# Kernel optimization log

Hardware: AMD Instinct MI355X
Metric: run time of the kernel (lower is better)

The kernel has to match this reference:

```python
import jax, jax.numpy as jnp
import numpy as np

DIM = 384
KEY_DIM = 32
NUM_HEADS = 8
ATTN_RATIO = 4
RESOLUTION = 48
N_TOKENS = RESOLUTION * RESOLUTION  # 2304
D_V = ATTN_RATIO * KEY_DIM          # 128
NH_KD = NUM_HEADS * KEY_DIM         # 256
DH = NUM_HEADS * D_V                # 1024
SCALE = KEY_DIM ** (-0.5)


def _make_bias_idxs(res):
    # offset (|dy|,|dx|) -> unique id via dy*res+dx (bijection onto 0..res^2-1)
    coords = np.stack(np.meshgrid(np.arange(res), np.arange(res), indexing='ij'), -1).reshape(-1, 2)
    off = np.abs(coords[:, None, :] - coords[None, :, :])  # (N,N,2)
    return (off[..., 0] * res + off[..., 1]).astype(np.int32)  # (N,N)


def setup_inputs() -> dict:
    key = jax.random.key(0)
    ks = jax.random.split(key, 12)
    f32 = jnp.float32
    x = jax.random.normal(ks[0], (N_TOKENS, DIM, 1, 1), dtype=f32)
    # 1x1 convs == linear layers: weight (out, in), bias (out,)
    q_w = jax.random.normal(ks[1], (NH_KD, DIM), dtype=f32) * 0.05
    q_b = jax.random.normal(ks[2], (NH_KD,), dtype=f32) * 0.02
    k_w = jax.random.normal(ks[3], (NH_KD, DIM), dtype=f32) * 0.05
    k_b = jax.random.normal(ks[4], (NH_KD,), dtype=f32) * 0.02
    v_w = jax.random.normal(ks[5], (DH, DIM), dtype=f32) * 0.05
    v_b = jax.random.normal(ks[6], (DH,), dtype=f32) * 0.02
    proj_w = jax.random.normal(ks[7], (DIM, DH), dtype=f32) * 0.05
    proj_b = jax.random.normal(ks[8], (DIM,), dtype=f32) * 0.02
    attention_biases = jax.random.normal(ks[9], (NUM_HEADS, 1, RESOLUTION * RESOLUTION), dtype=f32) * 0.02
    bias_idxs = jnp.asarray(_make_bias_idxs(RESOLUTION))  # (N,N) int32
    return {
        'x': x, 'q_w': q_w, 'q_b': q_b, 'k_w': k_w, 'k_b': k_b,
        'v_w': v_w, 'v_b': v_b, 'proj_w': proj_w, 'proj_b': proj_b,
        'attention_biases': attention_biases, 'bias_idxs': bias_idxs,
    }


def reference(x, q_w, q_b, k_w, k_b, v_w, v_b, proj_w, proj_b, attention_biases, bias_idxs):
    N = x.shape[0]
    xf = x.reshape(N, DIM)  # H=W=1 so 1x1 conv is a matmul
    q = (xf @ q_w.T + q_b).reshape(N, NUM_HEADS, KEY_DIM).transpose(1, 0, 2)  # (H,N,kd)
    k = (xf @ k_w.T + k_b).reshape(N, NUM_HEADS, KEY_DIM).transpose(1, 0, 2)  # (H,N,kd)
    v = (xf @ v_w.T + v_b).reshape(N, NUM_HEADS, D_V).transpose(1, 0, 2)      # (H,N,dv)
    bias = attention_biases[:, 0, :][:, bias_idxs]  # gather -> (H,N,N)
    attn = jnp.einsum('hnd,hmd->hnm', q, k) * SCALE + bias
    attn = jax.nn.softmax(attn, axis=-1)
    out = jnp.einsum('hnm,hmd->hnd', attn, v)       # (H,N,dv)
    out = out.transpose(1, 0, 2).reshape(N, DH)
    y = out @ proj_w.T + proj_b
    return y.reshape(N, DIM, 1, 1)
```

## Files before the change

kernel.cpp:

```cpp
#include <hip/hip_runtime.h>

typedef unsigned short u16;
typedef unsigned int u32;
typedef short bf16x8 __attribute__((ext_vector_type(8)));
typedef float f32x4 __attribute__((ext_vector_type(4)));

#define SCALE 0.17677669529663687f

static __device__ __forceinline__ float bf2f(u16 h) {
    u32 u = ((u32)h) << 16;
    float f;
    __builtin_memcpy(&f, &u, 4);
    return f;
}
static __device__ __forceinline__ u16 f2bf(float f) {
    u32 u;
    __builtin_memcpy(&u, &f, 4);
    u += 0x7fffu + ((u >> 16) & 1u);
    return (u16)(u >> 16);
}
static __device__ __forceinline__ float IN1(const void* p, int idx, int md) {
    return md ? ((const float*)p)[idx] : bf2f(((const u16*)p)[idx]);
}

__global__ void detect_kernel(const unsigned int* __restrict__ x, int* __restrict__ mode)
{
    int lane = threadIdx.x;
    int cnt = 0;
    for (int i = lane; i < 4096; i += 64) {
        unsigned int e = (x[i] >> 7) & 0xFFu;
        cnt += (e >= 100u && e <= 140u) ? 1 : 0;
    }
    for (int off = 32; off; off >>= 1) cnt += __shfl_down(cnt, off);
    if (lane == 0) *mode = (cnt < 2048) ? 1 : 0;
}

struct ConvArgs {
    const void* src[9];
    int ofs[10];
};
__global__ __launch_bounds__(256) void convert_all(
    ConvArgs a, u16* __restrict__ dst, const int* __restrict__ mode, int total)
{
    const int md = *mode;
    int base = (blockIdx.x * 256 + threadIdx.x) * 8;
    for (int e = 0; e < 8; e++) {
        int i = base + e;
        if (i >= total) return;
        int t = 0;
        for (int j = 1; j < 9; j++) t += (i >= a.ofs[j]) ? 1 : 0;
        int idx = i - a.ofs[t];
        dst[i] = md ? f2bf(((const float*)a.src[t])[idx])
                    : ((const u16*)a.src[t])[idx];
    }
}

__global__ __launch_bounds__(256) void qkv_kernel(
    const u16* __restrict__ x,
    const u16* __restrict__ qw, const u16* __restrict__ qb,
    const u16* __restrict__ kw, const u16* __restrict__ kb,
    const u16* __restrict__ vw, const u16* __restrict__ vb,
    u16* __restrict__ qo, u16* __restrict__ kT, u16* __restrict__ vTt)
{
    __shared__ __align__(16) short As[64 * 72];
    __shared__ __align__(16) short Bs[128 * 72];
    __shared__ __align__(16) short outS[128 * 72];
    const int tid  = threadIdx.x;
    const int lane = tid & 63;
    const int w    = tid >> 6;
    const int l15  = lane & 15, quad = lane >> 4;
    const int mT = blockIdx.y, nT = blockIdx.x;

    const u16* wp; const u16* bp; int r0, which;
    if (nT < 2)      { wp = qw; bp = qb; r0 = nT * 128;       which = 0; }
    else if (nT < 4) { wp = kw; bp = kb; r0 = (nT - 2) * 128; which = 1; }
    else             { wp = vw; bp = vb; r0 = (nT - 4) * 128; which = 2; }

    const int wm = (w >> 1) * 32, wn = (w & 1) * 64;
    const f32x4 vz = {0.f, 0.f, 0.f, 0.f};
    f32x4 acc[2][4];
    for (int mi = 0; mi < 2; mi++)
        for (int ni = 0; ni < 4; ni++) acc[mi][ni] = vz;

    const int arow = tid >> 2, aseg = tid & 3;
    const int brow = tid >> 1, bseg = tid & 1;

    for (int kk = 0; kk < 384; kk += 64) {
        for (int c = 0; c < 2; c++)
            *(bf16x8*)&As[arow * 72 + aseg * 16 + c * 8] =
                *(const bf16x8*)&x[(mT * 64 + arow) * 384 + kk + aseg * 16 + c * 8];
        for (int c = 0; c < 4; c++)
            *(bf16x8*)&Bs[brow * 72 + bseg * 32 + c * 8] =
                *(const bf16x8*)&wp[(r0 + brow) * 384 + kk + bseg * 32 + c * 8];
        __syncthreads();
        for (int s = 0; s < 2; s++) {
            bf16x8 af[2], bfr[4];
            for (int mi = 0; mi < 2; mi++)
                af[mi] = *(const bf16x8*)&As[(wm + mi * 16 + l15) * 72 + s * 32 + quad * 8];
            for (int ni = 0; ni < 4; ni++)
                bfr[ni] = *(const bf16x8*)&Bs[(wn + ni * 16 + l15) * 72 + s * 32 + quad * 8];
            for (int mi = 0; mi < 2; mi++)
                for (int ni = 0; ni < 4; ni++)
                    acc[mi][ni] = __builtin_amdgcn_mfma_f32_16x16x32_bf16(
                        af[mi], bfr[ni], acc[mi][ni], 0, 0, 0);
        }
        __syncthreads();
    }

    for (int ni = 0; ni < 4; ni++) {
        int colL = wn + ni * 16 + l15;
        float bias = bf2f(bp[r0 + colL]);
        for (int mi = 0; mi < 2; mi++) {
            int tokb = wm + mi * 16 + quad * 4;
            for (int rr = 0; rr < 4; rr++) {
                u16 val = f2bf(acc[mi][ni][rr] + bias);
                if (which == 2) outS[colL * 72 + tokb + rr] = val;
                else            outS[(tokb + rr) * 136 + colL] = val;
            }
        }
    }
    __syncthreads();

    if (which == 0) {
        for (int i = 0; i < 4; i++) {
            int c = tid + i * 256;
            int tok = c >> 4, seg = c & 15;
            *(bf16x8*)&qo[(mT * 64 + tok) * 256 + r0 + seg * 8] =
                *(const bf16x8*)&outS[tok * 136 + seg * 8];
        }
    } else if (which == 1) {
        int h0 = r0 >> 5;
        for (int i = 0; i < 4; i++) {
            int c = tid + i * 256;
            int tile = c >> 6, ln = c & 63;
            int head_loc = tile >> 2, t16_loc = tile & 3;
            int q2 = ln >> 4, l2 = ln & 15;
            *(bf16x8*)&kT[(((h0 + head_loc) * 144 + mT * 4 + t16_loc) << 9) + ln * 8] =
                *(const bf16x8*)&outS[(t16_loc * 16 + l2) * 136 + head_loc * 32 + q2 * 8];
        }
    } else {
        int hv = r0 >> 7;
        for (int i = 0; i < 4; i++) {
            int c = tid + i * 256;
            int tile = c >> 6, ln = c & 63;
            int kt_loc = tile >> 3, vb2 = tile & 7;
            int q2 = ln >> 4, l2 = ln & 15;
            *(bf16x8*)&vTt[(((hv * 72 + mT * 2 + kt_loc) * 8 + vb2) << 9) + ln * 8] =
                *(const bf16x8*)&outS[(vb2 * 16 + l2) * 72 + kt_loc * 32 + q2 * 8];
        }
    }
}

__global__ __launch_bounds__(256) void attn_v6(
    const u16* __restrict__ qbuf, const u16* __restrict__ kT,
    const u16* __restrict__ vTt,  const void* __restrict__ ab,
    u16* __restrict__ obuf, const int* __restrict__ mode)
{
    __shared__ __align__(16) float abl[2304];
    __shared__ __align__(16) u16   Pl[4][2][640];
    __shared__ __align__(16) float osh[2048];
    __shared__ __align__(16) float lsh[16];

    const int tid  = threadIdx.x;
    const int lane = tid & 63;
    const int w    = tid >> 6;
    const int l15  = lane & 15, quad = lane >> 4;
    const int head = blockIdx.y;
    const int q0   = blockIdx.x * 16;
    const int md   = *mode;

    for (int i = tid; i < 2304; i += 256) abl[i] = IN1(ab, head * 2304 + i, md);
    for (int i = tid; i < 2048; i += 256) osh[i] = 0.f;
    if (tid < 16) lsh[tid] = 0.f;
    __syncthreads();

    bf16x8 qfrag = *(const bf16x8*)&qbuf[(q0 + l15) * 256 + head * 32 + quad * 8];

    int qr[4], qc[4];
    for (int r = 0; r < 4; r++) {
        int qrow = q0 + quad * 4 + r;
        qr[r] = qrow / 48; qc[r] = qrow % 48;
    }

    const f32x4 vz = {0.f, 0.f, 0.f, 0.f};
    f32x4 o[8];
    for (int vb = 0; vb < 8; vb++) o[vb] = vz;
    float ls[4] = {0.f, 0.f, 0.f, 0.f};

    const int kstart = w * 576;
    const u16* kTb = kT  + head * 73728;
    const u16* vTb = vTt + head * 294912;
    const int t16 = kstart >> 4;
    const int vt0 = kstart >> 5;

    auto score_step = [&](int tt, bf16x8 a0, bf16x8 a1) {
        int kb = kstart + tt * 32;
        f32x4 s0 = __builtin_amdgcn_mfma_f32_16x16x32_bf16(qfrag, a0, vz, 0, 0, 0);
        f32x4 s1 = __builtin_amdgcn_mfma_f32_16x16x32_bf16(qfrag, a1, vz, 0, 0, 0);
        int k0 = kb + l15, k1 = k0 + 16;
        int kr0 = k0 / 48, kc0 = k0 % 48;
        int kr1 = k1 / 48, kc1 = k1 % 48;
        u16* P = &Pl[w][tt & 1][0];
        for (int r = 0; r < 4; r++) {
            float a0f = s0[r] * SCALE + abl[abs(qr[r] - kr0) * 48 + abs(qc[r] - kc0)];
            a0f = fminf(fmaxf(a0f, -60.f), 60.f);
            float p0 = __expf(a0f);
            ls[r] += p0;
            P[(quad * 4 + r) * 40 + l15] = f2bf(p0);
            float a1f = s1[r] * SCALE + abl[abs(qr[r] - kr1) * 48 + abs(qc[r] - kc1)];
            a1f = fminf(fmaxf(a1f, -60.f), 60.f);
            float p1 = __expf(a1f);
            ls[r] += p1;
            P[(quad * 4 + r) * 40 + 16 + l15] = f2bf(p1);
        }
    };

    {
        bf16x8 c0 = *(const bf16x8*)&kTb[((t16 + 0) * 64 + lane) * 8];
        bf16x8 c1 = *(const bf16x8*)&kTb[((t16 + 1) * 64 + lane) * 8];
        score_step(0, c0, c1);
    }
    bf16x8 kA0 = *(const bf16x8*)&kTb[((t16 + 2) * 64 + lane) * 8];
    bf16x8 kA1 = *(const bf16x8*)&kTb[((t16 + 3) * 64 + lane) * 8];

    for (int t = 0; t < 18; t++) {
        bf16x8 pf = *(const bf16x8*)&Pl[w][t & 1][l15 * 40 + quad * 8];

        bf16x8 vf[8];
        for (int vb = 0; vb < 8; vb++)
            vf[vb] = *(const bf16x8*)&vTb[(((vt0 + t) * 8 + vb) * 64 + lane) * 8];

        if (t < 17) {
            int nt = (t + 2 <= 17) ? (t + 2) : 17;
            bf16x8 kB0 = *(const bf16x8*)&kTb[((t16 + nt * 2) * 64 + lane) * 8];
            bf16x8 kB1 = *(const bf16x8*)&kTb[((t16 + nt * 2 + 1) * 64 + lane) * 8];
            score_step(t + 1, kA0, kA1);
            kA0 = kB0; kA1 = kB1;
        }

        for (int vb = 0; vb < 8; vb++)
            o[vb] = __builtin_amdgcn_mfma_f32_16x16x32_bf16(pf, vf[vb], o[vb], 0, 0, 0);
    }

    for (int r = 0; r < 4; r++)
        for (int off = 1; off < 16; off <<= 1)
            ls[r] += __shfl_xor(ls[r], off);

    for (int ph = 0; ph < 4; ph++) {
        if (w == ph) {
            for (int vb = 0; vb < 8; vb++)
                for (int r = 0; r < 4; r++)
                    osh[(quad * 4 + r) * 128 + vb * 16 + l15] += o[vb][r];
            if (l15 == 0)
                for (int r = 0; r < 4; r++) lsh[quad * 4 + r] += ls[r];
        }
        __syncthreads();
    }

    for (int i = tid; i < 2048; i += 256) {
        int row = i >> 7, dv = i & 127;
        obuf[(q0 + row) * 1024 + head * 128 + dv] = f2bf(osh[i] / lsh[row]);
    }
}

__global__ __launch_bounds__(256) void proj_kernel(
    const u16* __restrict__ ob, const u16* __restrict__ pw,
    const u16* __restrict__ pb, void* __restrict__ y, const int* __restrict__ mode)
{
    __shared__ __align__(16) short As[64 * 136];
    __shared__ __align__(16) short Bs[64 * 136];
    const int tid  = threadIdx.x;
    const int lane = tid & 63;
    const int w    = tid >> 6;
    const int l15  = lane & 15, quad = lane >> 4;
    const int mT = blockIdx.y, nT = blockIdx.x;
    const int wm = (w >> 1) * 32, wn = (w & 1) * 32;
    const int md = *mode;

    const f32x4 vz = {0.f, 0.f, 0.f, 0.f};
    f32x4 acc[2][2];
    for (int mi = 0; mi < 2; mi++)
        for (int ni = 0; ni < 2; ni++) acc[mi][ni] = vz;

    const int row = tid >> 2, seg = tid & 3;
    for (int kk = 0; kk < 1024; kk += 128) {
        for (int c = 0; c < 4; c++) {
            *(bf16x8*)&As[row * 136 + seg * 32 + c * 8] =
                *(const bf16x8*)&ob[(mT * 64 + row) * 1024 + kk + seg * 32 + c * 8];
            *(bf16x8*)&Bs[row * 136 + seg * 32 + c * 8] =
                *(const bf16x8*)&pw[(nT * 64 + row) * 1024 + kk + seg * 32 + c * 8];
        }
        __syncthreads();
        for (int s = 0; s < 4; s++) {
            bf16x8 af[2], bfr[2];
            for (int mi = 0; mi < 2; mi++)
                af[mi] = *(const bf16x8*)&As[(wm + mi * 16 + l15) * 136 + s * 32 + quad * 8];
            for (int ni = 0; ni < 2; ni++)
                bfr[ni] = *(const bf16x8*)&Bs[(wn + ni * 16 + l15) * 136 + s * 32 + quad * 8];
            for (int mi = 0; mi < 2; mi++)
                for (int ni = 0; ni < 2; ni++)
                    acc[mi][ni] = __builtin_amdgcn_mfma_f32_16x16x32_bf16(
                        af[mi], bfr[ni], acc[mi][ni], 0, 0, 0);
        }
        __syncthreads();
    }

    for (int ni = 0; ni < 2; ni++) {
        int col = nT * 64 + wn + ni * 16 + l15;
        float bias = bf2f(pb[col]);
        for (int mi = 0; mi < 2; mi++) {
            int rowb = mT * 64 + wm + mi * 16 + quad * 4;
            for (int rr = 0; rr < 4; rr++) {
                float val = acc[mi][ni][rr] + bias;
                int idx = (rowb + rr) * 384 + col;
                if (md) ((float*)y)[idx] = val;
                else    ((u16*)y)[idx]   = f2bf(val);
            }
        }
    }
}

extern "C" void kernel_launch(void* const* d_in, const int* in_sizes, int n_in,
                              void* d_out, int out_size, void* d_ws, size_t ws_size,
                              hipStream_t stream)
{
    const void *x = 0, *qw = 0, *qb = 0, *kw = 0, *kb = 0;
    const void *vw = 0, *vb = 0, *pw = 0, *pb = 0, *ab = 0;
    void* scratch = 0;

    for (int i = 0; i < n_in; i++) {
        const void* p = d_in[i];
        switch (in_sizes[i]) {
            case 884736:  x  = p; break;
            case 98304:   if (!qw) qw = p; else kw = p; break;
            case 256:     if (!qb) qb = p; else kb = p; break;
            case 393216:  if (!vw) vw = p; else pw = p; break;
            case 1024:    vb = p; break;
            case 384:     pb = p; break;
            case 18432:   ab = p; break;
            case 5308416: scratch = (void*)p; break;
        }
    }
    if (!scratch) scratch = d_ws;

    u16* arena = (u16*)scratch;
    u16* cx  = arena;
    u16* cqw = arena + 884736;
    u16* cqb = arena + 983040;
    u16* ckw = arena + 983296;
    u16* ckb = arena + 1081600;
    u16* cvw = arena + 1081856;
    u16* cvb = arena + 1475072;
    u16* cpw = arena + 1476096;
    u16* cpb = arena + 1869312;
    u16* q_bf = arena + 1869696;
    u16* kT   = arena + 2459520;
    u16* vTt  = arena + 3049344;
    u16* ob   = arena + 7767936;
    int* mode = ((int*)scratch) + 5308400;

    detect_kernel<<<1, 64, 0, stream>>>((const unsigned int*)x, mode);

    ConvArgs ca;
    ca.src[0] = x;  ca.src[1] = qw; ca.src[2] = qb; ca.src[3] = kw; ca.src[4] = kb;
    ca.src[5] = vw; ca.src[6] = vb; ca.src[7] = pw; ca.src[8] = pb;
    ca.ofs[0] = 0;       ca.ofs[1] = 884736;  ca.ofs[2] = 983040;
    ca.ofs[3] = 983296;  ca.ofs[4] = 1081600; ca.ofs[5] = 1081856;
    ca.ofs[6] = 1475072; ca.ofs[7] = 1476096; ca.ofs[8] = 1869312;
    ca.ofs[9] = 1869696;
    convert_all<<<(1869696 / 8 + 255) / 256, 256, 0, stream>>>(ca, arena, mode, 1869696);

    qkv_kernel<<<dim3(12, 36), 256, 0, stream>>>(cx, cqw, cqb, ckw, ckb, cvw, cvb,
                                                 q_bf, kT, vTt);
    attn_v6<<<dim3(144, 8), 256, 0, stream>>>(q_bf, kT, vTt, ab, ob, mode);
    proj_kernel<<<dim3(6, 36), 256, 0, stream>>>(ob, cpw, cpb, d_out, mode);
}
```

Baseline: 171.4 us.

## Fold dtype detection into convert, double-buffer QKV GEMM, use exp2 softmax

Removes the separate detect kernel by having every convert block recompute the dtype check on the first 1024 words of x, with block 0 writing the mode flag for later kernels. Double-buffers the QKV GEMM's LDS tiles through register prefetch so global loads overlap the MFMAs, with one barrier per k-step instead of two. In attention, the bias table is stored as bf16 pre-scaled by log2e and the score exponent uses exp2 with a folded scale, dropping the clamp. This saves a launch and softmax ALU work, at the cost of extra LDS, slightly lower bias precision, and possible overflow without the clamp since no max is subtracted.

```diff
diff --git a/kernel.cpp b/kernel.cpp
--- a/kernel.cpp
+++ b/kernel.cpp
@@ -5,7 +5,14 @@
 typedef short bf16x8 __attribute__((ext_vector_type(8)));
 typedef float f32x4 __attribute__((ext_vector_type(4)));
 
-#define SCALE 0.17677669529663687f
+#define SCALE2 0.25505413f
+#define LOG2E  1.4426950408889634f
+
+#if __has_builtin(__builtin_amdgcn_exp2f)
+#define EXP2(x) __builtin_amdgcn_exp2f(x)
+#else
+#define EXP2(x) exp2f(x)
+#endif
 
 static __device__ __forceinline__ float bf2f(u16 h) {
     u32 u = ((u32)h) << 16;
@@ -23,26 +30,28 @@
     return md ? ((const float*)p)[idx] : bf2f(((const u16*)p)[idx]);
 }
 
-__global__ void detect_kernel(const unsigned int* __restrict__ x, int* __restrict__ mode)
-{
-    int lane = threadIdx.x;
-    int cnt = 0;
-    for (int i = lane; i < 4096; i += 64) {
-        unsigned int e = (x[i] >> 7) & 0xFFu;
-        cnt += (e >= 100u && e <= 140u) ? 1 : 0;
-    }
-    for (int off = 32; off; off >>= 1) cnt += __shfl_down(cnt, off);
-    if (lane == 0) *mode = (cnt < 2048) ? 1 : 0;
-}
-
 struct ConvArgs {
     const void* src[9];
     int ofs[10];
 };
 __global__ __launch_bounds__(256) void convert_all(
-    ConvArgs a, u16* __restrict__ dst, const int* __restrict__ mode, int total)
-{
-    const int md = *mode;
+    ConvArgs a, u16* __restrict__ dst, int* __restrict__ mode_out, int total)
+{
+    __shared__ int cnt_sh;
+    if (threadIdx.x == 0) cnt_sh = 0;
+    __syncthreads();
+    const u32* xw = (const u32*)a.src[0];
+    int c = 0;
+    for (int i = threadIdx.x; i < 1024; i += 256) {
+        u32 e = (xw[i] >> 7) & 0xFFu;
+        c += (e >= 100u && e <= 140u) ? 1 : 0;
+    }
+    for (int off = 32; off; off >>= 1) c += __shfl_down(c, off);
+    if ((threadIdx.x & 63) == 0) atomicAdd(&cnt_sh, c);
+    __syncthreads();
+    const int md = (cnt_sh < 512) ? 1 : 0;
+    if (blockIdx.x == 0 && threadIdx.x == 0) *mode_out = md;
+
     int base = (blockIdx.x * 256 + threadIdx.x) * 8;
     for (int e = 0; e < 8; e++) {
         int i = base + e;
@@ -62,8 +71,8 @@
     const u16* __restrict__ vw, const u16* __restrict__ vb,
     u16* __restrict__ qo, u16* __restrict__ kT, u16* __restrict__ vTt)
 {
-    __shared__ __align__(16) short As[64 * 72];
-    __shared__ __align__(16) short Bs[128 * 72];
+    __shared__ __align__(16) short As[2][64 * 72];
+    __shared__ __align__(16) short Bs[2][128 * 72];
     __shared__ __align__(16) short outS[128 * 72];
     const int tid  = threadIdx.x;
     const int lane = tid & 63;
@@ -85,27 +94,44 @@
     const int arow = tid >> 2, aseg = tid & 3;
     const int brow = tid >> 1, bseg = tid & 1;
 
-    for (int kk = 0; kk < 384; kk += 64) {
+    bf16x8 ra[2], rb[4];
+    auto load_tile = [&](int kk) {
         for (int c = 0; c < 2; c++)
-            *(bf16x8*)&As[arow * 72 + aseg * 16 + c * 8] =
-                *(const bf16x8*)&x[(mT * 64 + arow) * 384 + kk + aseg * 16 + c * 8];
+            ra[c] = *(const bf16x8*)&x[(mT * 64 + arow) * 384 + kk + aseg * 16 + c * 8];
         for (int c = 0; c < 4; c++)
-            *(bf16x8*)&Bs[brow * 72 + bseg * 32 + c * 8] =
-                *(const bf16x8*)&wp[(r0 + brow) * 384 + kk + bseg * 32 + c * 8];
-        __syncthreads();
+            rb[c] = *(const bf16x8*)&wp[(r0 + brow) * 384 + kk + bseg * 32 + c * 8];
+    };
+    auto store_tile = [&](int b) {
+        for (int c = 0; c < 2; c++)
+            *(bf16x8*)&As[b][arow * 72 + aseg * 16 + c * 8] = ra[c];
+        for (int c = 0; c < 4; c++)
+            *(bf16x8*)&Bs[b][brow * 72 + bseg * 32 + c * 8] = rb[c];
+    };
+
+    load_tile(0);
+    store_tile(0);
+    __syncthreads();
+
+    for (int t = 0; t < 6; t++) {
+        if (t < 5) load_tile((t + 1) * 64);
+        const int b = t & 1;
         for (int s = 0; s < 2; s++) {
             bf16x8 af[2], bfr[4];
             for (int mi = 0; mi < 2; mi++)
-                af[mi] = *(const bf16x8*)&As[(wm + mi * 16 + l15) * 72 + s * 32 + quad * 8];
+                af[mi] = *(const bf16x8*)&As[b][(wm + mi * 16 + l15) * 72 + s * 32 + quad * 8];
             for (int ni = 0; ni < 4; ni++)
-                bfr[ni] = *(const bf16x8*)&Bs[(wn + ni * 16 + l15) * 72 + s * 32 + quad * 8];
+                bfr[ni] = *(const bf16x8*)&Bs[b][(wn + ni * 16 + l15) * 72 + s * 32 + quad * 8];
             for (int mi = 0; mi < 2; mi++)
                 for (int ni = 0; ni < 4; ni++)
                     acc[mi][ni] = __builtin_amdgcn_mfma_f32_16x16x32_bf16(
                         af[mi], bfr[ni], acc[mi][ni], 0, 0, 0);
         }
-        __syncthreads();
-    }
+        if (t < 5) {
+            store_tile((t + 1) & 1);
+            __syncthreads();
+        }
+    }
+    __syncthreads();
 
     for (int ni = 0; ni < 4; ni++) {
         int colL = wn + ni * 16 + l15;
@@ -156,7 +182,7 @@
     const u16* __restrict__ vTt,  const void* __restrict__ ab,
     u16* __restrict__ obuf, const int* __restrict__ mode)
 {
-    __shared__ __align__(16) float abl[2304];
+    __shared__ __align__(16) u16   abl[2304];
     __shared__ __align__(16) u16   Pl[4][2][640];
     __shared__ __align__(16) float osh[2048];
     __shared__ __align__(16) float lsh[16];
@@ -169,7 +195,8 @@
     const int q0   = blockIdx.x * 16;
     const int md   = *mode;
 
-    for (int i = tid; i < 2304; i += 256) abl[i] = IN1(ab, head * 2304 + i, md);
+    for (int i = tid; i < 2304; i += 256)
+        abl[i] = f2bf(IN1(ab, head * 2304 + i, md) * LOG2E);
     for (int i = tid; i < 2048; i += 256) osh[i] = 0.f;
     if (tid < 16) lsh[tid] = 0.f;
     __syncthreads();
@@ -202,14 +229,10 @@
         int kr1 = k1 / 48, kc1 = k1 % 48;
         u16* P = &Pl[w][tt & 1][0];
         for (int r = 0; r < 4; r++) {
-            float a0f = s0[r] * SCALE + abl[abs(qr[r] - kr0) * 48 + abs(qc[r] - kc0)];
-            a0f = fminf(fmaxf(a0f, -60.f), 60.f);
-            float p0 = __expf(a0f);
+            float p0 = EXP2(s0[r] * SCALE2 + bf2f(abl[abs(qr[r] - kr0) * 48 + abs(qc[r] - kc0)]));
             ls[r] += p0;
             P[(quad * 4 + r) * 40 + l15] = f2bf(p0);
-            float a1f = s1[r] * SCALE + abl[abs(qr[r] - kr1) * 48 + abs(qc[r] - kc1)];
-            a1f = fminf(fmaxf(a1f, -60.f), 60.f);
-            float p1 = __expf(a1f);
+            float p1 = EXP2(s1[r] * SCALE2 + bf2f(abl[abs(qr[r] - kr1) * 48 + abs(qc[r] - kc1)]));
             ls[r] += p1;
             P[(quad * 4 + r) * 40 + 16 + l15] = f2bf(p1);
         }
@@ -359,8 +382,6 @@
     u16* ob   = arena + 7767936;
     int* mode = ((int*)scratch) + 5308400;
 
-    detect_kernel<<<1, 64, 0, stream>>>((const unsigned int*)x, mode);
-
     ConvArgs ca;
     ca.src[0] = x;  ca.src[1] = qw; ca.src[2] = qb; ca.src[3] = kw; ca.src[4] = kb;
     ca.src[5] = vw; ca.src[6] = vb; ca.src[7] = pw; ca.src[8] = pb;
```

New measurement: 160.7 us. -6.3%, faster.
